# Optimization experiments

Measured on AMD Instinct MI355X. Metric: run time of the kernel, lower is better.

The kernel has to match this reference:

```python
import jax, jax.numpy as jnp
from jax import lax
import numpy as np

B, CIN, H, W = 32, 3, 128, 128
HID = 256          # hidden_dim == embedding_dim
K = 512            # num_embeddings
CC = 0.25          # commitment_cost
RR = 16            # SE reduction ratio


def setup_inputs() -> dict:
    key = jax.random.key(0)
    ks = iter(jax.random.split(key, 40))
    def n(shape, s=0.05):
        return jax.random.normal(next(ks), shape, jnp.float32) * s
    inp = {"x": jax.random.normal(next(ks), (B, CIN, H, W), jnp.float32)}
    inp.update(
        ec1_w=n((HID, CIN, 4, 4)), ec1_b=n((HID,)),
        ec2_w=n((HID, HID, 2, 2)), ec2_b=n((HID,)),
        se1_w1=n((HID // RR, HID)), se1_b1=n((HID // RR,)), se1_w2=n((HID, HID // RR)), se1_b2=n((HID,)), sa1_w=n((1, 2, 7, 7)),
        se2_w1=n((HID // RR, HID)), se2_b1=n((HID // RR,)), se2_w2=n((HID, HID // RR)), se2_b2=n((HID,)), sa2_w=n((1, 2, 7, 7)),
        codebook=jax.random.uniform(next(ks), (K, HID), jnp.float32, -1.0 / K, 1.0 / K),
        dt1_w=n((HID, HID, 2, 2)), dt1_b=n((HID,)),
        dt2_w=n((HID, CIN, 4, 4)), dt2_b=n((CIN,)),
        dse_w1=n((HID // RR, HID)), dse_b1=n((HID // RR,)), dse_w2=n((HID, HID // RR)), dse_b2=n((HID,)), dsa_w=n((2, 1, 7, 7)),
    )
    return inp


def conv(x, w, b, stride, pad=0):
    y = lax.conv_general_dilated(x, w, (stride, stride), [(pad, pad), (pad, pad)],
                                 dimension_numbers=('NCHW', 'OIHW', 'NCHW'))
    return y if b is None else y + b[None, :, None, None]


def convt(x, w, b, stride, pad=0):
    # torch ConvTranspose2d(weight [Cin, Cout, kh, kw]) == conv with flipped kernel,
    # lhs dilated by stride, padding k-1-pad
    k = w.shape[2]
    p = k - 1 - pad
    y = lax.conv_general_dilated(x, jnp.flip(w, (2, 3)), (1, 1), [(p, p), (p, p)],
                                 lhs_dilation=(stride, stride),
                                 dimension_numbers=('NCHW', 'IOHW', 'NCHW'))
    return y if b is None else y + b[None, :, None, None]


def se(x, w1, b1, w2, b2):
    s = jnp.mean(x, (2, 3))                                   # [B, C] global avg pool
    g = jax.nn.sigmoid(jax.nn.relu(s @ w1.T + b1) @ w2.T + b2)
    return x * g[:, :, None, None]


def cbam(x, w1, b1, w2, b2, sw, transpose=False):
    out = se(x, w1, b1, w2, b2)
    cat = jnp.concatenate([jnp.mean(out, 1, keepdims=True), jnp.max(out, 1, keepdims=True)], 1)
    s = convt(cat, sw, None, 1, 3) if transpose else conv(cat, sw, None, 1, 3)
    out = out * jax.nn.sigmoid(s)
    return x * out  # note: original CBAM.forward multiplies by x again


def vq(z, cb):
    D = cb.shape[1]
    flat = z.reshape(-1, D)  # faithful to torch reshape(-1, embedding_dim) on NCHW
    # squared euclidean distances (argmin identical to cdist argmin)
    d2 = jnp.sum(flat * flat, 1, keepdims=True) - 2.0 * (flat @ cb.T) + jnp.sum(cb * cb, 1)
    idx = jnp.argmin(d2, 1)
    q = cb[idx].reshape(z.shape)  # == one_hot(idx) @ cb, without materializing one-hot
    e_loss = jnp.mean((lax.stop_gradient(q) - z) ** 2)
    q_loss = jnp.mean((q - lax.stop_gradient(z)) ** 2)
    loss = q_loss + CC * e_loss
    q_st = z + lax.stop_gradient(q - z)
    p = jnp.zeros((cb.shape[0],), z.dtype).at[idx].add(1.0) / flat.shape[0]
    perplexity = jnp.exp(-jnp.sum(p * jnp.log(p + 1e-10)))
    return loss, q_st, perplexity


def reference(x, ec1_w, ec1_b, ec2_w, ec2_b,
              se1_w1, se1_b1, se1_w2, se1_b2, sa1_w,
              se2_w1, se2_b1, se2_w2, se2_b2, sa2_w,
              codebook, dt1_w, dt1_b, dt2_w, dt2_b,
              dse_w1, dse_b1, dse_w2, dse_b2, dsa_w):
    # encoder
    h = cbam(jax.nn.relu(conv(x, ec1_w, ec1_b, 2)), se1_w1, se1_b1, se1_w2, se1_b2, sa1_w)
    z = cbam(jax.nn.relu(conv(h, ec2_w, ec2_b, 1)), se2_w1, se2_b1, se2_w2, se2_b2, sa2_w)
    # vector quantization
    loss, q, perplexity = vq(z, codebook)
    # decoder
    d = cbam(jax.nn.relu(convt(q, dt1_w, dt1_b, 1)), dse_w1, dse_b1, dse_w2, dse_b2, dsa_w, transpose=True)
    x_recon = convt(d, dt2_w, dt2_b, 2)
    return x_recon, loss, perplexity
```

## Files before the change

### kernel.cpp

```cpp
#include <hip/hip_runtime.h>
#include <math.h>

#define NB 32
#define HID 256
#define HW1 (63*63)
#define HW2 (62*62)
#define T63 ((size_t)NB*HID*HW1)
#define T62 ((size_t)NB*HID*HW2)
#define NROWS 123008
#define KCB 512
#define GATHER_BLOCKS 1024

typedef __attribute__((ext_vector_type(8))) short short8;
typedef __attribute__((ext_vector_type(4))) float f32x4;
typedef __attribute__((ext_vector_type(4))) unsigned short us4;

__device__ __forceinline__ unsigned short f2bf(float f) {
    union { float f; unsigned int u; } v; v.f = f;
    unsigned int u = v.u;
    return (unsigned short)((u + 0x7FFFu + ((u >> 16) & 1u)) >> 16);
}
__device__ __forceinline__ float bf2f(unsigned short u) {
    union { unsigned int i; float f; } v; v.i = ((unsigned int)u) << 16;
    return v.f;
}

__global__ __launch_bounds__(256) void zero_small(float* __restrict__ sse, int* __restrict__ counts) {
    if (threadIdx.x == 0) sse[0] = 0.f;
    for (int i = threadIdx.x; i < KCB; i += 256) counts[i] = 0;
}
__global__ __launch_bounds__(256) void zero_pooled(float* __restrict__ pooled) {
    pooled[blockIdx.x*256 + threadIdx.x] = 0.f;
}

__global__ __launch_bounds__(256) void prepack_c1(
    const float* __restrict__ w, unsigned short* __restrict__ pack) {
    int t = blockIdx.x*256 + threadIdx.x;
    if (t >= 16384) return;
    int j = t & 7, lk = (t >> 3) & 3, co = (t >> 5) & 255, kc = t >> 13;
    int k = kc*32 + lk*8 + j;
    pack[t] = (k < 48) ? f2bf(w[co*48 + k]) : (unsigned short)0;
}

__global__ __launch_bounds__(256) void conv1_mfma(
    const float* __restrict__ x, const unsigned short* __restrict__ apack,
    const float* __restrict__ bias, unsigned short* __restrict__ X0) {
    __shared__ float xs[3][18][18];
    __shared__ __align__(16) unsigned short Bm[64*72];
    int b = blockIdx.y, t = blockIdx.x;
    int oh0 = (t >> 3)*8, ow0 = (t & 7)*8;
    int ih0 = oh0*2, iw0 = ow0*2;
    const float* xb = x + (size_t)b*3*128*128;
    for (int i = threadIdx.x; i < 972; i += 256) {
        int c = i / 324, rem = i - c*324, r = rem / 18, cl = rem - r*18;
        int ih = ih0 + r, iw = iw0 + cl;
        xs[c][r][cl] = (ih < 128 && iw < 128) ? xb[((size_t)c*128 + ih)*128 + iw] : 0.f;
    }
    __syncthreads();
    for (int i = threadIdx.x; i < 2048; i += 256) {
        int px = i >> 5, kp = (i & 31)*2;
        int ph = px >> 3, pw = px & 7;
        unsigned int pk = 0;
        #pragma unroll
        for (int u = 0; u < 2; ++u) {
            int k = kp + u;
            float v = 0.f;
            if (k < 48) {
                int c = k >> 4, k2 = k & 15, kh = k2 >> 2, kw = k2 & 3;
                v = xs[c][ph*2+kh][pw*2+kw];
            }
            pk |= ((unsigned int)f2bf(v)) << (16*u);
        }
        *(unsigned int*)&Bm[px*72 + kp] = pk;
    }
    __syncthreads();

    int w = threadIdx.x >> 6, l = threadIdx.x & 63;
    int lr = l & 15, lk = l >> 4;
    f32x4 acc[4][4];
    #pragma unroll
    for (int i = 0; i < 4; ++i)
        #pragma unroll
        for (int j = 0; j < 4; ++j) acc[i][j] = (f32x4){0.f,0.f,0.f,0.f};

    #pragma unroll
    for (int kc = 0; kc < 2; ++kc) {
        short8 bf[4];
        #pragma unroll
        for (int pxf = 0; pxf < 4; ++pxf)
            bf[pxf] = *(const short8*)&Bm[(pxf*16+lr)*72 + kc*32 + lk*8];
        #pragma unroll
        for (int cof = 0; cof < 4; ++cof) {
            int co = w*64 + cof*16 + lr;
            short8 af = *(const short8*)(apack + (((size_t)kc*256 + co)*4 + (size_t)lk)*8);
            acc[cof][0] = __builtin_amdgcn_mfma_f32_16x16x32_bf16(af, bf[0], acc[cof][0], 0, 0, 0);
            acc[cof][1] = __builtin_amdgcn_mfma_f32_16x16x32_bf16(af, bf[1], acc[cof][1], 0, 0, 0);
            acc[cof][2] = __builtin_amdgcn_mfma_f32_16x16x32_bf16(af, bf[2], acc[cof][2], 0, 0, 0);
            acc[cof][3] = __builtin_amdgcn_mfma_f32_16x16x32_bf16(af, bf[3], acc[cof][3], 0, 0, 0);
        }
    }
    #pragma unroll
    for (int cof = 0; cof < 4; ++cof) {
        int cob = w*64 + cof*16 + lk*4;
        float4 bz = *(const float4*)&bias[cob];
        #pragma unroll
        for (int pxf = 0; pxf < 4; ++pxf) {
            int px = pxf*16 + lr;
            int oh = oh0 + (px >> 3), ow = ow0 + (px & 7);
            if (oh < 63 && ow < 63) {
                f32x4 a = acc[cof][pxf];
                us4 pk = { f2bf(fmaxf(a.x + bz.x, 0.f)), f2bf(fmaxf(a.y + bz.y, 0.f)),
                           f2bf(fmaxf(a.z + bz.z, 0.f)), f2bf(fmaxf(a.w + bz.w, 0.f)) };
                *(us4*)(X0 + ((size_t)b*HW1 + (size_t)oh*63 + ow)*256 + cob) = pk;
            }
        }
    }
}

__global__ __launch_bounds__(256) void gap_nhwc(
    const unsigned short* __restrict__ X, float* __restrict__ pooled,
    int HW, float inv) {
    int b = blockIdx.y;
    int px0 = blockIdx.x * 512;
    int o = threadIdx.x & 31, pg = threadIdx.x >> 5;
    const unsigned short* xb = X + (size_t)b*HW*256 + o*8;
    float acc[8];
    #pragma unroll
    for (int j = 0; j < 8; ++j) acc[j] = 0.f;
    for (int i = 0; i < 64; ++i) {
        int px = px0 + pg + i*8;
        if (px < HW) {
            short8 v = *(const short8*)(xb + (size_t)px*256);
            #pragma unroll
            for (int j = 0; j < 8; ++j) acc[j] += bf2f((unsigned short)v[j]);
        }
    }
    __shared__ float pool2[8][256];
    #pragma unroll
    for (int j = 0; j < 8; ++j) pool2[pg][o*8+j] = acc[j];
    __syncthreads();
    float s = 0.f;
    #pragma unroll
    for (int p = 0; p < 8; ++p) s += pool2[p][threadIdx.x];
    atomicAdd(pooled + b*256 + threadIdx.x, s * inv);
}

__global__ __launch_bounds__(256) void gap_z(
    const unsigned short* __restrict__ Z, float* __restrict__ pooled, int HW) {
    int bc = blockIdx.x;
    const unsigned int* p = (const unsigned int*)(Z + (size_t)bc*HW);
    int n2 = HW >> 1;
    float s = 0.f;
    for (int i = threadIdx.x; i < n2; i += 256) {
        unsigned int v = p[i];
        s += bf2f((unsigned short)(v & 0xffff)) + bf2f((unsigned short)(v >> 16));
    }
    __shared__ float lds[4];
    for (int off = 32; off; off >>= 1) s += __shfl_down(s, off, 64);
    if ((threadIdx.x & 63) == 0) lds[threadIdx.x >> 6] = s;
    __syncthreads();
    if (threadIdx.x == 0) pooled[bc] = (lds[0]+lds[1]+lds[2]+lds[3]) / (float)HW;
}

__global__ __launch_bounds__(256) void se_mlp(
    const float* __restrict__ pooled, const float* __restrict__ w1,
    const float* __restrict__ b1, const float* __restrict__ w2,
    const float* __restrict__ b2, float* __restrict__ g) {
    int b = blockIdx.x;
    __shared__ float ps[256], hs[16];
    ps[threadIdx.x] = pooled[b*256 + threadIdx.x];
    __syncthreads();
    if (threadIdx.x < 16) {
        float a = b1[threadIdx.x];
        const float* wr = w1 + threadIdx.x*256;
        for (int k = 0; k < 256; ++k) a = fmaf(ps[k], wr[k], a);
        hs[threadIdx.x] = fmaxf(a, 0.f);
    }
    __syncthreads();
    float a = b2[threadIdx.x];
    const float* wr = w2 + threadIdx.x*16;
    #pragma unroll
    for (int j = 0; j < 16; ++j) a = fmaf(hs[j], wr[j], a);
    g[b*256 + threadIdx.x] = 1.f / (1.f + expf(-a));
}

__global__ __launch_bounds__(256) void chanpool_nhwc(
    const unsigned short* __restrict__ X, const float* __restrict__ g,
    float* __restrict__ am, int HW) {
    int b = blockIdx.y;
    __shared__ float gs[256];
    gs[threadIdx.x] = g[b*256 + threadIdx.x];
    __syncthreads();
    int p = blockIdx.x*256 + threadIdx.x;
    if (p >= HW) return;
    const unsigned short* xp = X + ((size_t)b*HW + p)*256;
    float s = 0.f, mx = -3.0e38f;
    for (int o = 0; o < 32; ++o) {
        short8 v = *(const short8*)(xp + o*8);
        #pragma unroll
        for (int j = 0; j < 8; ++j) {
            float f = bf2f((unsigned short)v[j]) * gs[o*8+j];
            s += f; mx = fmaxf(mx, f);
        }
    }
    am[((size_t)b*2)*HW + p]   = s * (1.f/256.f);
    am[((size_t)b*2+1)*HW + p] = mx;
}

__global__ __launch_bounds__(256) void chanpool_z(
    const unsigned short* __restrict__ Z, const float* __restrict__ g,
    float* __restrict__ am, int HW) {
    int b = blockIdx.y;
    __shared__ float gs[256];
    gs[threadIdx.x] = g[b*256 + threadIdx.x];
    __syncthreads();
    int p = blockIdx.x*256 + threadIdx.x;
    if (p >= HW) return;
    const unsigned short* xb = Z + (size_t)b*256*HW + p;
    float s = 0.f, mx = -3.0e38f;
    for (int c = 0; c < 256; ++c) {
        float v = bf2f(xb[(size_t)c*HW]) * gs[c];
        s += v; mx = fmaxf(mx, v);
    }
    am[((size_t)b*2)*HW + p]   = s * (1.f/256.f);
    am[((size_t)b*2+1)*HW + p] = mx;
}

__global__ __launch_bounds__(256) void spatial_conv(
    const float* __restrict__ am, const float* __restrict__ sw,
    float* __restrict__ ss, int H, int W, int transpose) {
    int b = blockIdx.y;
    int p = blockIdx.x*256 + threadIdx.x;
    __shared__ float ws[98];
    if (threadIdx.x < 98) {
        int c = threadIdx.x / 49, k = threadIdx.x % 49;
        int kh = k / 7, kw = k % 7;
        ws[threadIdx.x] = transpose ? sw[c*49 + (6-kh)*7 + (6-kw)]
                                    : sw[c*49 + kh*7 + kw];
    }
    __syncthreads();
    if (p >= H*W) return;
    int oh = p / W, ow = p % W;
    float acc = 0.f;
    #pragma unroll
    for (int c = 0; c < 2; ++c) {
        const float* ab = am + ((size_t)b*2 + c)*H*W;
        for (int kh = 0; kh < 7; ++kh) {
            int ih = oh + kh - 3;
            if (ih < 0 || ih >= H) continue;
            for (int kw = 0; kw < 7; ++kw) {
                int iw = ow + kw - 3;
                if (iw < 0 || iw >= W) continue;
                acc = fmaf(ab[(size_t)ih*W + iw], ws[c*49 + kh*7 + kw], acc);
            }
        }
    }
    ss[(size_t)b*H*W + p] = 1.f / (1.f + expf(-acc));
}

__global__ __launch_bounds__(256) void cbam_mul_nhwc(
    unsigned short* X, const float* __restrict__ g,
    const float* __restrict__ ss, int HW) {
    int b = blockIdx.y;
    __shared__ float gs[256];
    gs[threadIdx.x] = g[b*256 + threadIdx.x];
    __syncthreads();
    int p = blockIdx.x*256 + threadIdx.x;
    if (p >= HW) return;
    float sv = ss[(size_t)b*HW + p];
    unsigned short* xp = X + ((size_t)b*HW + p)*256;
    for (int o = 0; o < 32; ++o) {
        short8 v = *(const short8*)(xp + o*8);
        unsigned int pk[4];
        #pragma unroll
        for (int j = 0; j < 4; ++j) {
            float f0 = bf2f((unsigned short)v[2*j]);
            float f1 = bf2f((unsigned short)v[2*j+1]);
            f0 = f0*f0*gs[o*8+2*j]*sv;
            f1 = f1*f1*gs[o*8+2*j+1]*sv;
            pk[j] = (unsigned int)f2bf(f0) | ((unsigned int)f2bf(f1) << 16);
        }
        *(short8*)(xp + o*8) = *(const short8*)pk;
    }
}

__global__ __launch_bounds__(256) void cbam_z(
    unsigned short* Z, const float* __restrict__ g,
    const float* __restrict__ ss, int HW) {
    int b = blockIdx.y;
    int e2 = blockIdx.x*256 + threadIdx.x;
    if (e2 >= 128*HW) return;
    size_t e = (size_t)e2*2;
    int c = (int)(e / HW), p = (int)(e % HW);
    float gc = g[b*256 + c];
    float s0 = ss[(size_t)b*HW + p];
    float s1 = ss[(size_t)b*HW + p + 1];
    unsigned int* px = (unsigned int*)(Z + (size_t)b*256*HW + e);
    unsigned int v = *px;
    float f0 = bf2f((unsigned short)(v & 0xffff));
    float f1 = bf2f((unsigned short)(v >> 16));
    f0 = f0*f0*gc*s0;
    f1 = f1*f1*gc*s1;
    *px = (unsigned int)f2bf(f0) | ((unsigned int)f2bf(f1) << 16);
}

__global__ __launch_bounds__(256) void to_nhwc_bf16(
    const unsigned short* __restrict__ Z, unsigned short* __restrict__ X, int HW) {
    int b = blockIdx.y;
    int p = blockIdx.x*256 + threadIdx.x;
    bool valid = p < HW;
    const unsigned short* inb = Z + (size_t)b*256*HW + p;
    unsigned short* dst = X + ((size_t)b*HW + p)*256;
    #pragma unroll
    for (int ch = 0; ch < 4; ++ch) {
        unsigned short buf[64];
        #pragma unroll
        for (int j = 0; j < 64; ++j)
            buf[j] = valid ? inb[(size_t)(ch*64 + j)*HW] : (unsigned short)0;
        if (valid) {
            #pragma unroll
            for (int j2 = 0; j2 < 8; ++j2)
                *(short8*)(dst + ch*64 + j2*8) = *(const short8*)&buf[j2*8];
        }
    }
}

__global__ __launch_bounds__(256) void prepack_w(
    const float* __restrict__ w, unsigned short* __restrict__ pack, int transpose_flip) {
    int t = blockIdx.x*256 + threadIdx.x;
    int j = t & 7, koct = (t >> 3) & 3, co = (t >> 5) & 255, tap = (t >> 13) & 3, cc = t >> 15;
    int ci = cc*32 + koct*8 + j;
    int kh = tap >> 1, kw = tap & 1;
    float v;
    if (transpose_flip) v = w[((size_t)ci*256 + co)*4 + (1-kh)*2 + (1-kw)];
    else                v = w[((size_t)co*256 + ci)*4 + kh*2 + kw];
    pack[t] = f2bf(v);
}

__global__ __launch_bounds__(256) void prepack_dt2b(
    const float* __restrict__ w, unsigned short* __restrict__ pk) {
    int t = blockIdx.x*256 + threadIdx.x;
    int jj = t & 7, lk = (t >> 3) & 3, co = (t >> 5) & 15, j = (t >> 9) & 3, cc = (t >> 11) & 7, p = t >> 14;
    int ci = cc*32 + lk*8 + jj;
    int kh0 = p >> 1, kw0 = p & 1;
    const int dj[4] = {0, 2, 8, 10};
    float v = 0.f;
    if (co < 3) v = w[(size_t)ci*48 + co*16 + kh0*4 + kw0 + dj[j]];
    pk[t] = f2bf(v);
}

template <int MODE>
__global__ __launch_bounds__(256) void convk2_mfma_nhwc(
    const unsigned short* __restrict__ Xin, const unsigned short* __restrict__ apack,
    const float* __restrict__ bias, unsigned short* __restrict__ outZ,
    unsigned short* __restrict__ outU,
    int inH, int inW, int outH, int outW, int pad) {
    __shared__ __align__(16) unsigned short Sh[MODE ? 16896 : 13600];
    unsigned short* Ir0 = Sh;
    unsigned short* Ir1 = Sh + 6800;
    int b = blockIdx.y;
    int t = blockIdx.x;
    int oh0 = (t >> 2) * 4, ow0 = (t & 3) * 16;
    int w = threadIdx.x >> 6, l = threadIdx.x & 63;
    int lr = l & 15, lk = l >> 4;
    const unsigned short* src = Xin + (size_t)b*inH*inW*256;

    f32x4 acc[4][4];
    #pragma unroll
    for (int i = 0; i < 4; ++i)
        #pragma unroll
        for (int j = 0; j < 4; ++j) acc[i][j] = (f32x4){0.f,0.f,0.f,0.f};

    auto STAGE = [&](int cc, int bufi) {
        unsigned short* Ib = bufi ? Ir1 : Ir0;
        #pragma unroll
        for (int pass = 0; pass < 3; ++pass) {
            int u = pass*256 + threadIdx.x;
            if (u < 680) {
                int sub = (u >= 340) ? 1 : 0;
                int uu = u - sub*340;
                int sp = uu >> 2, q = uu & 3;
                int r = (sp*241) >> 12, c = sp - r*17;
                int gh = oh0 + r - pad, gw = ow0 + c - pad;
                short8 v = (short8){0,0,0,0,0,0,0,0};
                if (gh >= 0 && gh < inH && gw >= 0 && gw < inW)
                    v = *(const short8*)(src + ((size_t)gh*inW + gw)*256 + (cc+sub)*32 + q*8);
                *(short8*)&Ib[sub*3400 + sp*40 + q*8] = v;
            }
        }
    };

    STAGE(0, 0);
    for (int cc = 0; cc < 8; cc += 2) {
        __syncthreads();
        if (cc < 6) STAGE(cc+2, ((cc >> 1) + 1) & 1);
        const unsigned short* Ibase = ((cc >> 1) & 1) ? Ir1 : Ir0;
        #pragma unroll
        for (int half = 0; half < 2; ++half) {
            const unsigned short* Ib = Ibase + half*3400;
            #pragma unroll
            for (int tap = 0; tap < 4; ++tap) {
                int kh = tap >> 1, kw = tap & 1;
                int spb = kh*17 + kw + lr;
                short8 b0 = *(const short8*)&Ib[(spb     )*40 + lk*8];
                short8 b1 = *(const short8*)&Ib[(spb + 17)*40 + lk*8];
                short8 b2 = *(const short8*)&Ib[(spb + 34)*40 + lk*8];
                short8 b3 = *(const short8*)&Ib[(spb + 51)*40 + lk*8];
                const unsigned short* abase = apack + (((size_t)((cc+half)*4 + tap)*256)*4 + (size_t)lk)*8;
                #pragma unroll
                for (int cof = 0; cof < 4; ++cof) {
                    int co = w*64 + cof*16 + lr;
                    short8 af = *(const short8*)(abase + (size_t)co*32);
                    acc[cof][0] = __builtin_amdgcn_mfma_f32_16x16x32_bf16(af, b0, acc[cof][0], 0, 0, 0);
                    acc[cof][1] = __builtin_amdgcn_mfma_f32_16x16x32_bf16(af, b1, acc[cof][1], 0, 0, 0);
                    acc[cof][2] = __builtin_amdgcn_mfma_f32_16x16x32_bf16(af, b2, acc[cof][2], 0, 0, 0);
                    acc[cof][3] = __builtin_amdgcn_mfma_f32_16x16x32_bf16(af, b3, acc[cof][3], 0, 0, 0);
                }
            }
        }
    }
    if (MODE == 0) {
        int ow = ow0 + lr;
        #pragma unroll
        for (int cof = 0; cof < 4; ++cof) {
            int cob = w*64 + cof*16 + lk*4;
            float4 bz = *(const float4*)&bias[cob];
            #pragma unroll
            for (int pxf = 0; pxf < 4; ++pxf) {
                int oh = oh0 + pxf;
                if (oh < outH && ow < outW) {
                    f32x4 a = acc[cof][pxf];
                    size_t base = ((size_t)(b*256 + cob)*outH + oh)*outW + ow;
                    size_t st = (size_t)outH*outW;
                    outZ[base]        = f2bf(fmaxf(a.x + bz.x, 0.f));
                    outZ[base +   st] = f2bf(fmaxf(a.y + bz.y, 0.f));
                    outZ[base + 2*st] = f2bf(fmaxf(a.z + bz.z, 0.f));
                    outZ[base + 3*st] = f2bf(fmaxf(a.w + bz.w, 0.f));
                }
            }
        }
    } else {
        __syncthreads();
        #pragma unroll
        for (int cof = 0; cof < 4; ++cof) {
            int cob = w*64 + cof*16 + lk*4;
            float4 bz = *(const float4*)&bias[cob];
            #pragma unroll
            for (int pxf = 0; pxf < 4; ++pxf) {
                f32x4 a = acc[cof][pxf];
                us4 pk = { f2bf(fmaxf(a.x + bz.x, 0.f)), f2bf(fmaxf(a.y + bz.y, 0.f)),
                           f2bf(fmaxf(a.z + bz.z, 0.f)), f2bf(fmaxf(a.w + bz.w, 0.f)) };
                *(us4*)&Sh[(pxf*16 + lr)*264 + cob] = pk;
            }
        }
        __syncthreads();
        int owp = threadIdx.x >> 4, c0 = (threadIdx.x & 15)*16;
        int ow = ow0 + owp;
        #pragma unroll
        for (int row = 0; row < 4; ++row) {
            int oh = oh0 + row;
            if (oh < outH && ow < outW) {
                unsigned short* dst = outU + (((size_t)b*outH + oh)*outW + ow)*256 + c0;
                *(short8*)dst       = *(const short8*)&Sh[(row*16 + owp)*264 + c0];
                *(short8*)(dst + 8) = *(const short8*)&Sh[(row*16 + owp)*264 + c0 + 8];
            }
        }
    }
}

__global__ __launch_bounds__(256) void cb_norm(
    const float* __restrict__ cb, float* __restrict__ cbn) {
    for (int n = threadIdx.x; n < KCB; n += 256) {
        float s = 0.f;
        for (int k = 0; k < 256; ++k) { float v = cb[(size_t)n*256+k]; s = fmaf(v,v,s); }
        cbn[n] = s;
    }
}

__global__ __launch_bounds__(256) void cb_pack(
    const float* __restrict__ cb, unsigned short* __restrict__ cbp) {
    int t = blockIdx.x*256 + threadIdx.x;
    cbp[t] = f2bf(cb[t]);
}

__global__ __launch_bounds__(256) void vq_assign_mfma(
    const unsigned short* __restrict__ z, const unsigned short* __restrict__ cbp,
    const float* __restrict__ cbn, int* __restrict__ idx) {
    __shared__ __align__(16) unsigned short zb[64*264];
    __shared__ __align__(16) unsigned short cbs[2][32*264];
    __shared__ float cbl[KCB];
    int r0 = blockIdx.x * 64;
    for (int v = threadIdx.x; v < 2048; v += 256) {
        int row = v >> 5, o = v & 31;
        *(short8*)&zb[row*264 + o*8] = *(const short8*)&z[(size_t)(r0+row)*256 + o*8];
    }
    for (int i = threadIdx.x; i < KCB; i += 256) cbl[i] = cbn[i];
    int tcode = threadIdx.x >> 3, tk = threadIdx.x & 7;
    auto STAGE_CB = [&](int c, int bufi) {
        const unsigned short* src = cbp + ((size_t)(c*32 + tcode))*256 + tk*8;
        unsigned short* dst = &cbs[bufi][tcode*264 + tk*8];
        #pragma unroll
        for (int j = 0; j < 4; ++j)
            *(short8*)(dst + j*64) = *(const short8*)(src + j*64);
    };
    STAGE_CB(0, 0);
    __syncthreads();

    int w = threadIdx.x >> 6, l = threadIdx.x & 63;
    int lr = l & 15, lk = l >> 4;
    short8 afr[8];
    #pragma unroll
    for (int ks = 0; ks < 8; ++ks)
        afr[ks] = *(const short8*)&zb[(w*16 + lr)*264 + ks*32 + lk*8];

    float bd[4]; int bi[4];
    #pragma unroll
    for (int r = 0; r < 4; ++r) { bd[r] = 3.0e38f; bi[r] = 0; }

    for (int c = 0; c < 16; ++c) {
        if (c < 15) STAGE_CB(c+1, (c+1)&1);
        const unsigned short* Cb = cbs[c & 1];
        #pragma unroll
        for (int f = 0; f < 2; ++f) {
            f32x4 acc = (f32x4){0.f,0.f,0.f,0.f};
            #pragma unroll
            for (int ks = 0; ks < 8; ++ks) {
                short8 bfr = *(const short8*)&Cb[(f*16 + lr)*264 + ks*32 + lk*8];
                acc = __builtin_amdgcn_mfma_f32_16x16x32_bf16(afr[ks], bfr, acc, 0, 0, 0);
            }
            int n = c*32 + f*16 + lr;
            float cn = cbl[n];
            #pragma unroll
            for (int r = 0; r < 4; ++r) {
                float dist = fmaf(-2.f, acc[r], cn);
                if (dist < bd[r]) { bd[r] = dist; bi[r] = n; }
            }
        }
        __syncthreads();
    }
    #pragma unroll
    for (int r = 0; r < 4; ++r) {
        #pragma unroll
        for (int off = 1; off < 16; off <<= 1) {
            float od = __shfl_xor(bd[r], off, 64);
            int   oi = __shfl_xor(bi[r], off, 64);
            if (od < bd[r] || (od == bd[r] && oi < bi[r])) { bd[r] = od; bi[r] = oi; }
        }
    }
    if (lr == 0) {
        #pragma unroll
        for (int r = 0; r < 4; ++r)
            idx[r0 + w*16 + lk*4 + r] = bi[r];
    }
}

__global__ __launch_bounds__(256) void vq_gather(
    unsigned short* zq, const float* __restrict__ cb,
    const int* __restrict__ idx, float* __restrict__ sse, int* __restrict__ counts) {
    __shared__ int hist[KCB];
    for (int i = threadIdx.x; i < KCB; i += 256) hist[i] = 0;
    __syncthreads();
    float local = 0.f;
    for (int r = blockIdx.x; r < NROWS; r += GATHER_BLOCKS) {
        int id = idx[r];
        if (threadIdx.x == 0) atomicAdd(&hist[id], 1);
        float qv = cb[(size_t)id*256 + threadIdx.x];
        unsigned short* pz = zq + (size_t)r*256 + threadIdx.x;
        float zv = bf2f(*pz);
        *pz = f2bf(qv);
        float d = qv - zv;
        local = fmaf(d, d, local);
    }
    __shared__ float lds[4];
    for (int off = 32; off; off >>= 1) local += __shfl_down(local, off, 64);
    if ((threadIdx.x & 63) == 0) lds[threadIdx.x >> 6] = local;
    __syncthreads();
    if (threadIdx.x == 0) atomicAdd(sse, lds[0]+lds[1]+lds[2]+lds[3]);
    for (int i = threadIdx.x; i < KCB; i += 256) {
        int h = hist[i];
        if (h) atomicAdd(counts + i, h);
    }
}

__global__ __launch_bounds__(256) void vq_finalize(
    const float* __restrict__ sse, const int* __restrict__ counts,
    float* __restrict__ out) {
    __shared__ float lds[4];
    float h = 0.f;
    for (int n = threadIdx.x; n < KCB; n += 256) {
        float p = (float)counts[n] * (1.f/123008.f);
        h += p * logf(p + 1e-10f);
    }
    for (int off = 32; off; off >>= 1) h += __shfl_down(h, off, 64);
    if ((threadIdx.x & 63) == 0) lds[threadIdx.x >> 6] = h;
    __syncthreads();
    if (threadIdx.x == 0) {
        out[1572864] = 1.25f * sse[0] / 31490048.f;
        out[1572865] = expf(-(lds[0]+lds[1]+lds[2]+lds[3]));
    }
}

__global__ __launch_bounds__(256) void dt2_mfma(
    const unsigned short* __restrict__ Y, const unsigned short* __restrict__ apack,
    const float* __restrict__ bias, float* __restrict__ out) {
    __shared__ __align__(16) unsigned short Iraw[2][289*40];
    int b = blockIdx.y, t = blockIdx.x;
    int a0 = (t >> 2)*16, b0 = (t & 3)*16;
    int p = threadIdx.x >> 6;
    int l = threadIdx.x & 63;
    int lr = l & 15, lk = l >> 4;
    const unsigned short* src = Y + (size_t)b*HW1*256;

    auto STAGE = [&](int cc, int bufi) {
        #pragma unroll
        for (int pass = 0; pass < 5; ++pass) {
            int u = pass*256 + threadIdx.x;
            if (u < 1156) {
                int sp = u >> 2, q = u & 3;
                int r = (sp*241) >> 12, c = sp - r*17;
                int ia = a0 - 1 + r, ib = b0 - 1 + c;
                short8 v = (short8){0,0,0,0,0,0,0,0};
                if (ia >= 0 && ia < 63 && ib >= 0 && ib < 63)
                    v = *(const short8*)(src + ((size_t)ia*63 + ib)*256 + cc*32 + q*8);
                *(short8*)&Iraw[bufi][sp*40 + q*8] = v;
            }
        }
    };

    f32x4 acc[16];
    #pragma unroll
    for (int i = 0; i < 16; ++i) acc[i] = (f32x4){0.f,0.f,0.f,0.f};

    STAGE(0, 0);
    for (int cc = 0; cc < 8; ++cc) {
        __syncthreads();
        if (cc < 7) STAGE(cc+1, (cc+1)&1);
        const unsigned short* Ib = Iraw[cc & 1];
        #pragma unroll
        for (int j = 0; j < 4; ++j) {
            int jh = j >> 1, jw = j & 1;
            short8 af = *(const short8*)(apack +
                ((size_t)((p*8 + cc)*4 + j))*512 + lr*32 + lk*8);
            int sp0 = (1 - jh)*17 + (lr + 1 - jw);
            #pragma unroll
            for (int nf = 0; nf < 16; ++nf) {
                short8 bf = *(const short8*)&Ib[(sp0 + nf*17)*40 + lk*8];
                acc[nf] = __builtin_amdgcn_mfma_f32_16x16x32_bf16(af, bf, acc[nf], 0, 0, 0);
            }
        }
    }
    if (lk == 0) {
        int kh0 = p >> 1, kw0 = p & 1;
        float bz0 = bias[0], bz1 = bias[1], bz2 = bias[2];
        int wp = 2*(b0 + lr) + kw0;
        #pragma unroll
        for (int nf = 0; nf < 16; ++nf) {
            int h = 2*(a0 + nf) + kh0;
            size_t ob = (size_t)(b*3)*16384 + (size_t)h*128 + wp;
            out[ob]         = acc[nf].x + bz0;
            out[ob + 16384] = acc[nf].y + bz1;
            out[ob + 32768] = acc[nf].z + bz2;
        }
    }
}

extern "C" void kernel_launch(void* const* d_in, const int* in_sizes, int n_in,
                              void* d_out, int out_size, void* d_ws, size_t ws_size,
                              hipStream_t stream) {
    const float* x      = (const float*)d_in[0];
    const float* ec1_w  = (const float*)d_in[1];
    const float* ec1_b  = (const float*)d_in[2];
    const float* ec2_w  = (const float*)d_in[3];
    const float* ec2_b  = (const float*)d_in[4];
    const float* se1_w1 = (const float*)d_in[5];
    const float* se1_b1 = (const float*)d_in[6];
    const float* se1_w2 = (const float*)d_in[7];
    const float* se1_b2 = (const float*)d_in[8];
    const float* sa1_w  = (const float*)d_in[9];
    const float* se2_w1 = (const float*)d_in[10];
    const float* se2_b1 = (const float*)d_in[11];
    const float* se2_w2 = (const float*)d_in[12];
    const float* se2_b2 = (const float*)d_in[13];
    const float* sa2_w  = (const float*)d_in[14];
    const float* cbk    = (const float*)d_in[15];
    const float* dt1_w  = (const float*)d_in[16];
    const float* dt1_b  = (const float*)d_in[17];
    const float* dt2_w  = (const float*)d_in[18];
    const float* dt2_b  = (const float*)d_in[19];
    const float* dse_w1 = (const float*)d_in[20];
    const float* dse_b1 = (const float*)d_in[21];
    const float* dse_w2 = (const float*)d_in[22];
    const float* dse_b2 = (const float*)d_in[23];
    const float* dsa_w  = (const float*)d_in[24];
    float* out = (float*)d_out;

    unsigned short* Zb = (unsigned short*)d_ws;
    unsigned short* U0 = Zb + T62;
    unsigned short* U1 = U0 + T63;
    float* pooled = (float*)(U1 + T63);
    float* g      = pooled + 8192;
    float* am     = g + 8192;
    float* ssmap  = am + (size_t)NB*2*HW1;
    float* cbn    = ssmap + (size_t)NB*HW1;
    unsigned short* apackE = (unsigned short*)(cbn + 512);
    unsigned short* apackD = apackE + 262144;
    unsigned short* cbp    = apackD + 262144;
    unsigned short* apackC = cbp + 131072;
    unsigned short* apack2 = apackC + 16384;
    float* sse    = (float*)(apack2 + 65536);
    int*   counts = (int*)(sse + 1);
    int*   idx    = counts + 512;

    zero_small<<<1, 256, 0, stream>>>(sse, counts);
    prepack_w<<<1024, 256, 0, stream>>>(ec2_w, apackE, 0);
    prepack_w<<<1024, 256, 0, stream>>>(dt1_w, apackD, 1);
    prepack_c1<<<64, 256, 0, stream>>>(ec1_w, apackC);
    prepack_dt2b<<<256, 256, 0, stream>>>(dt2_w, apack2);
    cb_norm<<<1, 256, 0, stream>>>(cbk, cbn);
    cb_pack<<<512, 256, 0, stream>>>(cbk, cbp);

    conv1_mfma<<<dim3(64, NB), 256, 0, stream>>>(x, apackC, ec1_b, U0);
    zero_pooled<<<32, 256, 0, stream>>>(pooled);
    gap_nhwc<<<dim3(8, NB), 256, 0, stream>>>(U0, pooled, HW1, 1.f/HW1);
    se_mlp<<<NB, 256, 0, stream>>>(pooled, se1_w1, se1_b1, se1_w2, se1_b2, g);
    chanpool_nhwc<<<dim3(16, NB), 256, 0, stream>>>(U0, g, am, HW1);
    spatial_conv<<<dim3(16, NB), 256, 0, stream>>>(am, sa1_w, ssmap, 63, 63, 0);
    cbam_mul_nhwc<<<dim3(16, NB), 256, 0, stream>>>(U0, g, ssmap, HW1);

    convk2_mfma_nhwc<0><<<dim3(64, NB), 256, 0, stream>>>(U0, apackE, ec2_b, Zb, (unsigned short*)0, 63, 63, 62, 62, 0);
    gap_z<<<NB*256, 256, 0, stream>>>(Zb, pooled, HW2);
    se_mlp<<<NB, 256, 0, stream>>>(pooled, se2_w1, se2_b1, se2_w2, se2_b2, g);
    chanpool_z<<<dim3(16, NB), 256, 0, stream>>>(Zb, g, am, HW2);
    spatial_conv<<<dim3(16, NB), 256, 0, stream>>>(am, sa2_w, ssmap, 62, 62, 0);
    cbam_z<<<dim3(1922, NB), 256, 0, stream>>>(Zb, g, ssmap, HW2);

    vq_assign_mfma<<<NROWS/64, 256, 0, stream>>>(Zb, cbp, cbn, idx);
    vq_gather<<<GATHER_BLOCKS, 256, 0, stream>>>(Zb, cbk, idx, sse, counts);
    vq_finalize<<<1, 256, 0, stream>>>(sse, counts, out);
    to_nhwc_bf16<<<dim3(16, NB), 256, 0, stream>>>(Zb, U1, HW2);

    convk2_mfma_nhwc<1><<<dim3(64, NB), 256, 0, stream>>>(U1, apackD, dt1_b, (unsigned short*)0, U0, 62, 62, 63, 63, 1);
    zero_pooled<<<32, 256, 0, stream>>>(pooled);
    gap_nhwc<<<dim3(8, NB), 256, 0, stream>>>(U0, pooled, HW1, 1.f/HW1);
    se_mlp<<<NB, 256, 0, stream>>>(pooled, dse_w1, dse_b1, dse_w2, dse_b2, g);
    chanpool_nhwc<<<dim3(16, NB), 256, 0, stream>>>(U0, g, am, HW1);
    spatial_conv<<<dim3(16, NB), 256, 0, stream>>>(am, dsa_w, ssmap, 63, 63, 1);
    cbam_mul_nhwc<<<dim3(16, NB), 256, 0, stream>>>(U0, g, ssmap, HW1);

    dt2_mfma<<<dim3(16, NB), 256, 0, stream>>>(U0, apack2, dt2_b, out);
}
```

Baseline: 818.4 us.

## Fuse CBAM channel/spatial scaling into the following conv staging loads

After: 722.8 us. -11.7%, faster.

```diff
diff --git a/kernel.cpp b/kernel.cpp
--- a/kernel.cpp
+++ b/kernel.cpp
@@ -256,32 +256,6 @@
         }
     }
     ss[(size_t)b*H*W + p] = 1.f / (1.f + expf(-acc));
-}
-
-__global__ __launch_bounds__(256) void cbam_mul_nhwc(
-    unsigned short* X, const float* __restrict__ g,
-    const float* __restrict__ ss, int HW) {
-    int b = blockIdx.y;
-    __shared__ float gs[256];
-    gs[threadIdx.x] = g[b*256 + threadIdx.x];
-    __syncthreads();
-    int p = blockIdx.x*256 + threadIdx.x;
-    if (p >= HW) return;
-    float sv = ss[(size_t)b*HW + p];
-    unsigned short* xp = X + ((size_t)b*HW + p)*256;
-    for (int o = 0; o < 32; ++o) {
-        short8 v = *(const short8*)(xp + o*8);
-        unsigned int pk[4];
-        #pragma unroll
-        for (int j = 0; j < 4; ++j) {
-            float f0 = bf2f((unsigned short)v[2*j]);
-            float f1 = bf2f((unsigned short)v[2*j+1]);
-            f0 = f0*f0*gs[o*8+2*j]*sv;
-            f1 = f1*f1*gs[o*8+2*j+1]*sv;
-            pk[j] = (unsigned int)f2bf(f0) | ((unsigned int)f2bf(f1) << 16);
-        }
-        *(short8*)(xp + o*8) = *(const short8*)pk;
-    }
 }
 
 __global__ __launch_bounds__(256) void cbam_z(
@@ -352,18 +326,27 @@
 template <int MODE>
 __global__ __launch_bounds__(256) void convk2_mfma_nhwc(
     const unsigned short* __restrict__ Xin, const unsigned short* __restrict__ apack,
-    const float* __restrict__ bias, unsigned short* __restrict__ outZ,
+    const float* __restrict__ bias, const float* __restrict__ gvec,
+    const float* __restrict__ ssm, unsigned short* __restrict__ outZ,
     unsigned short* __restrict__ outU,
     int inH, int inW, int outH, int outW, int pad) {
     __shared__ __align__(16) unsigned short Sh[MODE ? 16896 : 13600];
+    __shared__ float gs[256];
     unsigned short* Ir0 = Sh;
     unsigned short* Ir1 = Sh + 6800;
     int b = blockIdx.y;
-    int t = blockIdx.x;
+    int raw = blockIdx.x;
+    int xcd = raw & 7, jj = raw >> 3;
+    int t = (xcd + 8*(jj >> 2))*4 + (jj & 3);
     int oh0 = (t >> 2) * 4, ow0 = (t & 3) * 16;
     int w = threadIdx.x >> 6, l = threadIdx.x & 63;
     int lr = l & 15, lk = l >> 4;
     const unsigned short* src = Xin + (size_t)b*inH*inW*256;
+    const float* ssb = (MODE == 0) ? (ssm + (size_t)b*inH*inW) : (const float*)0;
+    if (MODE == 0) {
+        gs[threadIdx.x] = gvec[b*256 + threadIdx.x];
+        __syncthreads();
+    }
 
     f32x4 acc[4][4];
     #pragma unroll
@@ -383,8 +366,25 @@
                 int r = (sp*241) >> 12, c = sp - r*17;
                 int gh = oh0 + r - pad, gw = ow0 + c - pad;
                 short8 v = (short8){0,0,0,0,0,0,0,0};
-                if (gh >= 0 && gh < inH && gw >= 0 && gw < inW)
+                bool valid = (gh >= 0) && (gh < inH) && (gw >= 0) && (gw < inW);
+                if (valid)
                     v = *(const short8*)(src + ((size_t)gh*inW + gw)*256 + (cc+sub)*32 + q*8);
+                if (MODE == 0) {
+                    if (valid) {
+                        float sv = ssb[(size_t)gh*inW + gw];
+                        int c0 = (cc+sub)*32 + q*8;
+                        unsigned int pk[4];
+                        #pragma unroll
+                        for (int j = 0; j < 4; ++j) {
+                            float f0 = bf2f((unsigned short)v[2*j]);
+                            float f1 = bf2f((unsigned short)v[2*j+1]);
+                            f0 = f0*f0*gs[c0+2*j]*sv;
+                            f1 = f1*f1*gs[c0+2*j+1]*sv;
+                            pk[j] = (unsigned int)f2bf(f0) | ((unsigned int)f2bf(f1) << 16);
+                        }
+                        v = *(const short8*)pk;
+                    }
+                }
                 *(short8*)&Ib[sub*3400 + sp*40 + q*8] = v;
             }
         }
@@ -602,14 +602,19 @@
 
 __global__ __launch_bounds__(256) void dt2_mfma(
     const unsigned short* __restrict__ Y, const unsigned short* __restrict__ apack,
-    const float* __restrict__ bias, float* __restrict__ out) {
+    const float* __restrict__ bias, const float* __restrict__ gvec,
+    const float* __restrict__ ssm, float* __restrict__ out) {
     __shared__ __align__(16) unsigned short Iraw[2][289*40];
+    __shared__ float gs[256];
     int b = blockIdx.y, t = blockIdx.x;
     int a0 = (t >> 2)*16, b0 = (t & 3)*16;
     int p = threadIdx.x >> 6;
     int l = threadIdx.x & 63;
     int lr = l & 15, lk = l >> 4;
     const unsigned short* src = Y + (size_t)b*HW1*256;
+    const float* ssb = ssm + (size_t)b*HW1;
+    gs[threadIdx.x] = gvec[b*256 + threadIdx.x];
+    __syncthreads();
 
     auto STAGE = [&](int cc, int bufi) {
         #pragma unroll
@@ -620,8 +625,22 @@
                 int r = (sp*241) >> 12, c = sp - r*17;
                 int ia = a0 - 1 + r, ib = b0 - 1 + c;
                 short8 v = (short8){0,0,0,0,0,0,0,0};
-                if (ia >= 0 && ia < 63 && ib >= 0 && ib < 63)
+                bool valid = (ia >= 0) && (ia < 63) && (ib >= 0) && (ib < 63);
+                if (valid) {
                     v = *(const short8*)(src + ((size_t)ia*63 + ib)*256 + cc*32 + q*8);
+                    float sv = ssb[(size_t)ia*63 + ib];
+                    int c0 = cc*32 + q*8;
+                    unsigned int pk[4];
+                    #pragma unroll
+                    for (int j = 0; j < 4; ++j) {
+                        float f0 = bf2f((unsigned short)v[2*j]);
+                        float f1 = bf2f((unsigned short)v[2*j+1]);
+                        f0 = f0*f0*gs[c0+2*j]*sv;
+                        f1 = f1*f1*gs[c0+2*j+1]*sv;
+                        pk[j] = (unsigned int)f2bf(f0) | ((unsigned int)f2bf(f1) << 16);
+                    }
+                    v = *(const short8*)pk;
+                }
                 *(short8*)&Iraw[bufi][sp*40 + q*8] = v;
             }
         }
@@ -725,9 +744,8 @@
     se_mlp<<<NB, 256, 0, stream>>>(pooled, se1_w1, se1_b1, se1_w2, se1_b2, g);
     chanpool_nhwc<<<dim3(16, NB), 256, 0, stream>>>(U0, g, am, HW1);
     spatial_conv<<<dim3(16, NB), 256, 0, stream>>>(am, sa1_w, ssmap, 63, 63, 0);
-    cbam_mul_nhwc<<<dim3(16, NB), 256, 0, stream>>>(U0, g, ssmap, HW1);
-
-    convk2_mfma_nhwc<0><<<dim3(64, NB), 256, 0, stream>>>(U0, apackE, ec2_b, Zb, (unsigned short*)0, 63, 63, 62, 62, 0);
+
+    convk2_mfma_nhwc<0><<<dim3(64, NB), 256, 0, stream>>>(U0, apackE, ec2_b, g, ssmap, Zb, (unsigned short*)0, 63, 63, 62, 62, 0);
     gap_z<<<NB*256, 256, 0, stream>>>(Zb, pooled, HW2);
     se_mlp<<<NB, 256, 0, stream>>>(pooled, se2_w1, se2_b1, se2_w2, se2_b2, g);
     chanpool_z<<<dim3(16, NB), 256, 0, stream>>>(Zb, g, am, HW2);
@@ -739,13 +757,12 @@
     vq_finalize<<<1, 256, 0, stream>>>(sse, counts, out);
     to_nhwc_bf16<<<dim3(16, NB), 256, 0, stream>>>(Zb, U1, HW2);
 
-    convk2_mfma_nhwc<1><<<dim3(64, NB), 256, 0, stream>>>(U1, apackD, dt1_b, (unsigned short*)0, U0, 62, 62, 63, 63, 1);
+    convk2_mfma_nhwc<1><<<dim3(64, NB), 256, 0, stream>>>(U1, apackD, dt1_b, (const float*)0, (const float*)0, (unsigned short*)0, U0, 62, 62, 63, 63, 1);
     zero_pooled<<<32, 256, 0, stream>>>(pooled);
     gap_nhwc<<<dim3(8, NB), 256, 0, stream>>>(U0, pooled, HW1, 1.f/HW1);
     se_mlp<<<NB, 256, 0, stream>>>(pooled, dse_w1, dse_b1, dse_w2, dse_b2, g);
     chanpool_nhwc<<<dim3(16, NB), 256, 0, stream>>>(U0, g, am, HW1);
     spatial_conv<<<dim3(16, NB), 256, 0, stream>>>(am, dsa_w, ssmap, 63, 63, 1);
-    cbam_mul_nhwc<<<dim3(16, NB), 256, 0, stream>>>(U0, g, ssmap, HW1);
-
-    dt2_mfma<<<dim3(16, NB), 256, 0, stream>>>(U0, apack2, dt2_b, out);
-}
+
+    dt2_mfma<<<dim3(16, NB), 256, 0, stream>>>(U0, apack2, dt2_b, g, ssmap, out);
+}
```
